# Kernel optimization log

Measured on AMD Instinct MI355X. Metric: run time of the kernel, lower is better.

Reference implementation:

```python
import jax, jax.numpy as jnp
import numpy as np

NUM_LAYERS = 32
SELECT_K = 24
NUM_CHOICES = NUM_LAYERS - SELECT_K + 1  # 9
TAU = 1.0  # forward never calls _update_tau, so current_tau == initial_tau
EPS = 1e-10


def setup_inputs() -> dict:
    key = jax.random.key(0)
    k1, k2, k3 = jax.random.split(key, 3)
    B, L, D = 32, NUM_LAYERS, 4096
    all_features = jax.random.normal(k1, (B, L, D), dtype=jnp.float32)
    logits = jax.random.normal(k2, (NUM_CHOICES,), dtype=jnp.float32)
    uniform_noise = jax.random.uniform(k3, (B, NUM_CHOICES), dtype=jnp.float32)
    return {"all_features": all_features, "logits": logits, "uniform_noise": uniform_noise}


def gumbel_softmax_hard(logits_b, uniform_noise, tau):
    # logits_b: [B, C], uniform_noise: [B, C]
    g = -jnp.log(-jnp.log(uniform_noise + EPS) + EPS)  # Gumbel(0,1)
    y_soft = jax.nn.softmax((logits_b + g) / tau, axis=-1)
    idx = jnp.argmax(y_soft, axis=-1)
    y_hard = jax.nn.one_hot(idx, y_soft.shape[-1], dtype=y_soft.dtype)
    # straight-through estimator
    return y_hard + y_soft - jax.lax.stop_gradient(y_soft)


def reference(all_features, logits, uniform_noise):
    B = all_features.shape[0]
    expanded_logits = jnp.broadcast_to(logits[None, :], (B, NUM_CHOICES))
    selection_probs = gumbel_softmax_hard(expanded_logits, uniform_noise, TAU)  # [B, C]
    # overlapping windows: win_idx[c, k] = c + k
    win_idx = jnp.arange(NUM_CHOICES)[:, None] + jnp.arange(SELECT_K)[None, :]  # [C, K]
    windows = all_features[:, win_idx, :]  # [B, C, K, D]
    selected_features = jnp.einsum('bc,bckd->bkd', selection_probs, windows)  # [B, K, D]
    return selected_features, selection_probs
```

## Files before the change

### kernel.cpp

```cpp
#include <hip/hip_runtime.h>

#define N_LAYERS 32
#define SEL_K 24
#define N_CHOICES 9
#define BATCH 32
#define DIM 4096
#define G_EPS 1e-10f

__global__ __launch_bounds__(256) void layer_selector_kernel(
    const float* __restrict__ feat,
    const float* __restrict__ logits,
    const float* __restrict__ noise,
    float* __restrict__ out)
{
    const int bk = blockIdx.x;
    const int b = bk / SEL_K;
    const int k = bk % SEL_K;

    __shared__ int s_idx;
    __shared__ float s_p;
    __shared__ float s_probs[N_CHOICES];

    if (threadIdx.x == 0) {
        float x[N_CHOICES];
        float m = -1e30f;
        #pragma unroll
        for (int c = 0; c < N_CHOICES; ++c) {
            float u = noise[b * N_CHOICES + c];
            float g = -logf(-logf(u + G_EPS) + G_EPS);
            x[c] = logits[c] + g;
            m = fmaxf(m, x[c]);
        }
        float sum = 0.f;
        #pragma unroll
        for (int c = 0; c < N_CHOICES; ++c) {
            x[c] = expf(x[c] - m);
            sum += x[c];
        }
        int idx = 0;
        float best = -1.f;
        #pragma unroll
        for (int c = 0; c < N_CHOICES; ++c) {
            float y = x[c] / sum;
            if (y > best) { best = y; idx = c; }
        }
        s_idx = idx;
        s_p = (1.0f + best) - best;
        #pragma unroll
        for (int c = 0; c < N_CHOICES; ++c)
            s_probs[c] = (c == idx) ? s_p : 0.0f;
    }
    __syncthreads();

    const int idx = s_idx;
    const float p = s_p;

    const float4* __restrict__ src =
        (const float4*)(feat + ((size_t)b * N_LAYERS + (size_t)(idx + k)) * DIM);
    float4* __restrict__ dst =
        (float4*)(out + ((size_t)b * SEL_K + (size_t)k) * DIM);

    #pragma unroll
    for (int i = threadIdx.x; i < DIM / 4; i += 256) {
        float4 v = src[i];
        v.x *= p; v.y *= p; v.z *= p; v.w *= p;
        dst[i] = v;
    }

    if (k == 0 && threadIdx.x < N_CHOICES) {
        out[(size_t)BATCH * SEL_K * DIM + (size_t)b * N_CHOICES + threadIdx.x] =
            s_probs[threadIdx.x];
    }
}

extern "C" void kernel_launch(void* const* d_in, const int* in_sizes, int n_in,
                              void* d_out, int out_size, void* d_ws, size_t ws_size,
                              hipStream_t stream) {
    const float* feat   = (const float*)d_in[0];
    const float* logits = (const float*)d_in[1];
    const float* noise  = (const float*)d_in[2];
    float* out = (float*)d_out;

    dim3 grid(BATCH * SEL_K);
    dim3 block(256);
    hipLaunchKernelGGL(layer_selector_kernel, grid, block, 0, stream,
                       feat, logits, noise, out);
}
```

Baseline: 11.34 us.

## Split rows into half-chunks, compute selection per thread, use nontemporal stores

Each thread now computes the Gumbel-softmax selection itself, which removes the shared-memory handoff and the block barrier. The grid doubles so each block copies half a row, giving more blocks in flight and less work per block. Output writes use nontemporal stores to avoid polluting the cache. In exchange, every thread redundantly evaluates nine log/exp pairs, which adds latency before the copy can start.

```diff
diff --git a/kernel.cpp b/kernel.cpp
--- a/kernel.cpp
+++ b/kernel.cpp
@@ -6,6 +6,9 @@
 #define BATCH 32
 #define DIM 4096
 #define G_EPS 1e-10f
+#define CHUNKS 48
+
+typedef float vfloat4 __attribute__((ext_vector_type(4)));
 
 __global__ __launch_bounds__(256) void layer_selector_kernel(
     const float* __restrict__ feat,
@@ -13,63 +16,53 @@
     const float* __restrict__ noise,
     float* __restrict__ out)
 {
-    const int bk = blockIdx.x;
-    const int b = bk / SEL_K;
-    const int k = bk % SEL_K;
+    const int blk = blockIdx.x;
+    const int b = blk / CHUNKS;
+    const int chunk = blk % CHUNKS;
 
-    __shared__ int s_idx;
-    __shared__ float s_p;
-    __shared__ float s_probs[N_CHOICES];
+    float x[N_CHOICES];
+    float m = -1e30f;
+    #pragma unroll
+    for (int c = 0; c < N_CHOICES; ++c) {
+        float u = noise[b * N_CHOICES + c];
+        float g = -logf(-logf(u + G_EPS) + G_EPS);
+        x[c] = logits[c] + g;
+        m = fmaxf(m, x[c]);
+    }
+    float sum = 0.f;
+    #pragma unroll
+    for (int c = 0; c < N_CHOICES; ++c) {
+        x[c] = expf(x[c] - m);
+        sum += x[c];
+    }
+    int idx = 0;
+    float best = -1.f;
+    #pragma unroll
+    for (int c = 0; c < N_CHOICES; ++c) {
+        float y = x[c] / sum;
+        if (y > best) { best = y; idx = c; }
+    }
+    const float p = (1.0f + best) - best;
 
-    if (threadIdx.x == 0) {
-        float x[N_CHOICES];
-        float m = -1e30f;
-        #pragma unroll
-        for (int c = 0; c < N_CHOICES; ++c) {
-            float u = noise[b * N_CHOICES + c];
-            float g = -logf(-logf(u + G_EPS) + G_EPS);
-            x[c] = logits[c] + g;
-            m = fmaxf(m, x[c]);
-        }
-        float sum = 0.f;
-        #pragma unroll
-        for (int c = 0; c < N_CHOICES; ++c) {
-            x[c] = expf(x[c] - m);
-            sum += x[c];
-        }
-        int idx = 0;
-        float best = -1.f;
-        #pragma unroll
-        for (int c = 0; c < N_CHOICES; ++c) {
-            float y = x[c] / sum;
-            if (y > best) { best = y; idx = c; }
-        }
-        s_idx = idx;
-        s_p = (1.0f + best) - best;
-        #pragma unroll
-        for (int c = 0; c < N_CHOICES; ++c)
-            s_probs[c] = (c == idx) ? s_p : 0.0f;
-    }
-    __syncthreads();
+    const int k = chunk >> 1;
+    const int col4 = (chunk & 1) * (DIM / 8);
 
-    const int idx = s_idx;
-    const float p = s_p;
-
-    const float4* __restrict__ src =
-        (const float4*)(feat + ((size_t)b * N_LAYERS + (size_t)(idx + k)) * DIM);
-    float4* __restrict__ dst =
-        (float4*)(out + ((size_t)b * SEL_K + (size_t)k) * DIM);
+    const vfloat4* __restrict__ src =
+        (const vfloat4*)(feat + ((size_t)b * N_LAYERS + (size_t)(idx + k)) * DIM) + col4;
+    vfloat4* __restrict__ dst =
+        (vfloat4*)(out + ((size_t)b * SEL_K + (size_t)k) * DIM) + col4;
 
     #pragma unroll
-    for (int i = threadIdx.x; i < DIM / 4; i += 256) {
-        float4 v = src[i];
-        v.x *= p; v.y *= p; v.z *= p; v.w *= p;
-        dst[i] = v;
+    for (int i = threadIdx.x; i < DIM / 8; i += 256) {
+        vfloat4 v = src[i];
+        v *= p;
+        __builtin_nontemporal_store(v, &dst[i]);
     }
 
-    if (k == 0 && threadIdx.x < N_CHOICES) {
-        out[(size_t)BATCH * SEL_K * DIM + (size_t)b * N_CHOICES + threadIdx.x] =
-            s_probs[threadIdx.x];
+    if (chunk == 0 && threadIdx.x < N_CHOICES) {
+        const int c = threadIdx.x;
+        out[(size_t)BATCH * SEL_K * DIM + (size_t)b * N_CHOICES + c] =
+            (c == idx) ? p : 0.0f;
     }
 }
 
@@ -81,7 +74,7 @@
     const float* noise  = (const float*)d_in[2];
     float* out = (float*)d_out;
 
-    dim3 grid(BATCH * SEL_K);
+    dim3 grid(BATCH * CHUNKS);
     dim3 block(256);
     hipLaunchKernelGGL(layer_selector_kernel, grid, block, 0, stream,
                        feat, logits, noise, out);
```

New measurement: 11.44 us. No clear change (+0.9%).
